# Optimization experiments

Hardware: AMD Instinct MI355X
Metric: run time of the kernel (lower is better)

Reference implementation:

```python
import jax, jax.numpy as jnp
import numpy as np

B, D, H = 4096, 64, 1024  # batch, state dim, hidden width


def setup_inputs() -> dict:
    key = jax.random.key(0)
    ks = jax.random.split(key, 4)
    def w(k, shape, fan_in):
        return (jax.random.normal(k, shape, jnp.float32) / np.float32(np.sqrt(fan_in)))
    return {
        "x": jax.random.normal(ks[0], (B, 1 + D), jnp.float32),
        "W1": w(ks[1], (D, H), D),
        "b1": jnp.zeros((H,), jnp.float32),
        "W2": w(ks[2], (H, H), H),
        "b2": jnp.zeros((H,), jnp.float32),
        "W3": w(ks[3], (H, D), H),
        "b3": jnp.zeros((D,), jnp.float32),
    }


def _mlp(z, W1, b1, W2, b2, W3, b3):
    # tanh MLP vector field: d -> h -> h -> d
    h = jnp.tanh(z @ W1 + b1)
    h = jnp.tanh(h @ W2 + b2)
    return h @ W3 + b3


def reference(x, W1, b1, W2, b2, W3, b3):
    x_in = x[:, 1:]                        # [B, D] state (col 0 is logp channel)
    f = lambda z: _mlp(z, W1, b1, W2, b2, W3, b3)
    x_out = f(x_in)                        # [B, D]

    # Exact Jacobian trace: same math as the torch per-dim autograd.grad loop,
    # expressed as D forward-mode JVPs vmapped over the identity basis.
    eye = jnp.eye(x_in.shape[1], dtype=x.dtype)

    def diag_entry(e):                     # e: [D] basis vector
        _, t = jax.jvp(f, (x_in,), (jnp.broadcast_to(e, x_in.shape),))
        return t @ e                       # [B] = J[:, i, i]

    trJ = jnp.sum(jax.vmap(diag_entry)(eye), axis=0)  # [B]

    out = jnp.concatenate([-trJ[:, None], x_out], axis=1)  # [B, 1+D]
    return out + 0.0 * x  # faithful to `+ 0 * x` in the original
```

## Files before the change

kernel.cpp:

```cpp
#include <hip/hip_runtime.h>
#include <cmath>

typedef unsigned short u16;
typedef __attribute__((ext_vector_type(8))) short s8v;
typedef __attribute__((ext_vector_type(4))) float f4v;
typedef __attribute__((ext_vector_type(16))) float f16v;

__device__ __forceinline__ u16 f2bf(float f) {
    union { float f; unsigned u; } v; v.f = f;
    unsigned r = v.u + 0x7FFFu + ((v.u >> 16) & 1u);
    return (u16)(r >> 16);
}
__device__ __forceinline__ float tanh_fast(float x) {
    float e = __builtin_amdgcn_exp2f(x * 2.88539008177792681f);
    return 1.f - 2.f * __builtin_amdgcn_rcpf(1.f + e);
}
__device__ __forceinline__ int wslot(int row, int c) {
    return ((((c >> 2) << 6) | ((c & 3) << 4) | (row & 15)) ^ c);
}
__device__ __forceinline__ size_t fragoff(int n, int k) {
    return (((size_t)(n >> 5) * 64 + (k >> 4)) * 64 + (n & 31) + (((k >> 3) & 1) << 5)) * 8 + (k & 7);
}

__launch_bounds__(256)
__global__ void cnf_prep(const float* __restrict__ x, const float* __restrict__ W1,
                         const float* __restrict__ W2, const float* __restrict__ W3,
                         u16* __restrict__ W2Tf, u16* __restrict__ VTf,
                         u16* __restrict__ xb, u16* __restrict__ W1T,
                         u16* __restrict__ W3Tf, float* __restrict__ trJ)
{
    __shared__ float w2s[32][33];
    __shared__ float w1s[64][33];
    const int a = blockIdx.x * 32;
    const int b = blockIdx.y * 32;
    const int t = threadIdx.x;

    #pragma unroll
    for (int it = 0; it < 4; ++it) {
        int idx = t + it * 256;
        w2s[idx >> 5][idx & 31] = W2[(a + (idx >> 5)) * 1024 + b + (idx & 31)];
    }
    #pragma unroll
    for (int it = 0; it < 8; ++it) {
        int idx = t + it * 256;
        w1s[idx >> 5][idx & 31] = W1[(idx >> 5) * 1024 + a + (idx & 31)];
    }
    __syncthreads();

    #pragma unroll
    for (int it = 0; it < 4; ++it) {
        int idx = t + it * 256;
        int rr = idx >> 5, cc = idx & 31;
        W2Tf[fragoff(b + rr, a + cc)] = f2bf(w2s[cc][rr]);
    }
    #pragma unroll
    for (int it = 0; it < 4; ++it) {
        int idx = t + it * 256;
        int qq = idx >> 5, pp = idx & 31;
        const float* w3row = W3 + (b + qq) * 64;
        float u = 0.f;
        #pragma unroll
        for (int i4 = 0; i4 < 16; ++i4) {
            f4v w3v = *(const f4v*)&w3row[i4 * 4];
            u += w3v[0] * w1s[i4 * 4 + 0][pp] + w3v[1] * w1s[i4 * 4 + 1][pp]
               + w3v[2] * w1s[i4 * 4 + 2][pp] + w3v[3] * w1s[i4 * 4 + 3][pp];
        }
        VTf[fragoff(b + qq, a + pp)] = f2bf(w2s[pp][qq] * u);
    }
    {
        int bid = blockIdx.y * 32 + blockIdx.x;
        int e = bid * 256 + t;
        xb[e] = f2bf(x[(e >> 6) * 65 + 1 + (e & 63)]);
    }
    if (blockIdx.y == 0) {
        int pp = t >> 3, i0 = (t & 7) * 8;
        s8v v;
        #pragma unroll
        for (int j = 0; j < 8; ++j) v[j] = (short)f2bf(w1s[i0 + j][pp]);
        *(s8v*)&W1T[(a + pp) * 64 + i0] = v;
        if (t < 128) trJ[blockIdx.x * 128 + t] = 0.f;
    }
    if (blockIdx.y == 1) {
        int idx = blockIdx.x * 256 + t;
        int n = idx & 63, k0 = (idx >> 6) * 8;
        s8v v;
        #pragma unroll
        for (int j = 0; j < 8; ++j) v[j] = (short)f2bf(W3[(k0 + j) * 64 + n]);
        *(s8v*)&W3Tf[fragoff(n, k0)] = v;
    }
}

__launch_bounds__(256)
__global__ void cnf_gemm1(const u16* __restrict__ xb, const u16* __restrict__ W1T,
                          const float* __restrict__ b1,
                          u16* __restrict__ h1, u16* __restrict__ g1)
{
    __shared__ __align__(16) u16 lds[12 * 1024];
    __shared__ __align__(16) u16 hls[128 * 64];
    __shared__ __align__(16) u16 gls[128 * 64];
    const int t = threadIdx.x;
    const int wave = t >> 6, lane = t & 63;
    const int wm = wave >> 1, wn = wave & 1;
    const int g = lane >> 4, lr = lane & 15;
    const int arow0 = blockIdx.x * 128, bcol0 = blockIdx.y * 64;

    #pragma unroll
    for (int i = 0; i < 4; ++i) {
        int ch = t + i * 256, row = ch >> 3, c = ch & 7;
        *(s8v*)&lds[(row >> 4) * 1024 + wslot(row, c) * 8] =
            *(const s8v*)&xb[(arow0 + row) * 64 + c * 8];
    }
    #pragma unroll
    for (int i = 0; i < 2; ++i) {
        int ch = t + i * 256, row = ch >> 3, c = ch & 7;
        *(s8v*)&lds[(8 + (row >> 4)) * 1024 + wslot(row, c) * 8] =
            *(const s8v*)&W1T[(bcol0 + row) * 64 + c * 8];
    }
    __syncthreads();

    f4v acc[4][2];
    #pragma unroll
    for (int mi = 0; mi < 4; ++mi)
        #pragma unroll
        for (int ni = 0; ni < 2; ++ni) acc[mi][ni] = f4v{0.f,0.f,0.f,0.f};

    #pragma unroll
    for (int ks = 0; ks < 2; ++ks) {
        const int lo = (ks * 64 + (lane ^ ((ks * 4 + g) & 7))) * 8;
        s8v af[4], bf[2];
        #pragma unroll
        for (int mi = 0; mi < 4; ++mi) af[mi] = *(const s8v*)&lds[(wm * 4 + mi) * 1024 + lo];
        #pragma unroll
        for (int ni = 0; ni < 2; ++ni) bf[ni] = *(const s8v*)&lds[(8 + wn * 2 + ni) * 1024 + lo];
        #pragma unroll
        for (int mi = 0; mi < 4; ++mi)
            #pragma unroll
            for (int ni = 0; ni < 2; ++ni)
                acc[mi][ni] = __builtin_amdgcn_mfma_f32_16x16x32_bf16(af[mi], bf[ni], acc[mi][ni], 0, 0, 0);
    }

    #pragma unroll
    for (int mi = 0; mi < 4; ++mi) {
        const int rowl = wm * 64 + mi * 16 + g * 4;
        #pragma unroll
        for (int ni = 0; ni < 2; ++ni) {
            const int coll = wn * 32 + ni * 16 + lr;
            const float bv = b1[bcol0 + coll];
            const int cc = coll >> 3, jj = coll & 7;
            #pragma unroll
            for (int r = 0; r < 4; ++r) {
                const int row = rowl + r;
                float h = tanh_fast(acc[mi][ni][r] + bv);
                int idx = row * 64 + ((cc ^ (row & 7)) << 3) + jj;
                hls[idx] = f2bf(h);
                gls[idx] = f2bf(1.f - h * h);
            }
        }
    }
    __syncthreads();

    #pragma unroll
    for (int i = 0; i < 4; ++i) {
        int id = i * 256 + t;
        int row = id >> 3, ch = id & 7;
        int src = row * 64 + ((ch ^ (row & 7)) << 3);
        size_t dst = (size_t)(arow0 + row) * 1024 + bcol0 + ch * 8;
        *(s8v*)&h1[dst] = *(const s8v*)&hls[src];
        *(s8v*)&g1[dst] = *(const s8v*)&gls[src];
    }
}

#define LOADA(dh, dg, ko) \
    do { dh = *(const s8v*)(h1p + (ko)); dg = *(const s8v*)(g1p + (ko)); } while (0)

#define LOADB(B, kkg)                                                          \
    do { _Pragma("unroll")                                                     \
         for (int _ks = 0; _ks < 2; ++_ks)                                     \
         _Pragma("unroll")                                                     \
         for (int _ni = 0; _ni < 2; ++_ni) {                                   \
             size_t _o = (((size_t)(nt0 + _ni) * 64 + (kkg) * 2 + _ks) * 64 + lane) * 8; \
             B[_ks*4 + _ni*2 + 0] = *(const s8v*)&W2Tf[_o];                    \
             B[_ks*4 + _ni*2 + 1] = *(const s8v*)&VTf[_o];                     \
         } } while (0)

#define WRITEA(sh, sg, bb)                                                     \
    do { u16* _wb = &lds[bb][0];                                               \
         *(s8v*)&_wb[sdst] = sh; *(s8v*)&_wb[4096 + sdst] = sg; } while (0)

#define MIDBODY(kt, AwH, AwG, AlH, AlG, Bc, Bn)                                \
    {                                                                          \
        if ((kt) < 30) { const int _ko = ((kt) + 2) * 32; LOADA(AlH, AlG, _ko); } \
        if ((kt) < 31) { WRITEA(AwH, AwG, ((kt) + 1) & 1); LOADB(Bn, (kt) + 1); } \
        const u16* buf = &lds[(kt) & 1][0];                                    \
        _Pragma("unroll")                                                      \
        for (int ks = 0; ks < 2; ++ks) {                                       \
            const int lp = (lane ^ ((lane >> 5) << 2) ^ (ks << 1)) * 8;        \
            const int R = wrt * 2 + ks;                                        \
            s8v a1 = *(const s8v*)&buf[R * 512 + lp];                          \
            s8v a2 = *(const s8v*)&buf[4096 + R * 512 + lp];                   \
            _Pragma("unroll")                                                  \
            for (int ni = 0; ni < 2; ++ni) {                                   \
                acc1[ni] = __builtin_amdgcn_mfma_f32_32x32x16_bf16(a1, Bc[ks*4+ni*2+0], acc1[ni], 0, 0, 0); \
                acc2[ni] = __builtin_amdgcn_mfma_f32_32x32x16_bf16(a2, Bc[ks*4+ni*2+1], acc2[ni], 0, 0, 0); \
            }                                                                  \
        }                                                                      \
        __syncthreads();                                                       \
    }

__launch_bounds__(512, 2)
__global__ void cnf_mid(const u16* __restrict__ h1, const u16* __restrict__ g1,
                        const u16* __restrict__ W2Tf, const u16* __restrict__ VTf,
                        const float* __restrict__ b2,
                        u16* __restrict__ h2f, float* __restrict__ trJ)
{
    __shared__ __align__(16) u16 lds[2][8192];

    const int t = threadIdx.x;
    const int wave = t >> 6, lane = t & 63;
    const int wrt = wave & 3;
    const int wn  = wave >> 2;
    const int arow0 = blockIdx.x * 128;
    const int ntb = blockIdx.y * 4;
    const int nt0 = ntb + wn * 2;

    const int row = t >> 2, c = t & 3;
    const int R0 = (row >> 5) * 2 + (c >> 1);
    const int L0 = (row & 31) + ((c & 1) << 5);
    const int sdst = (R0 * 64 + (L0 ^ ((L0 >> 5) << 2) ^ ((R0 & 1) << 1))) * 8;
    const u16* h1p = h1 + (size_t)(arow0 + row) * 1024 + c * 8;
    const u16* g1p = g1 + (size_t)(arow0 + row) * 1024 + c * 8;

    f16v acc1[2], acc2[2];
    #pragma unroll
    for (int ni = 0; ni < 2; ++ni)
        #pragma unroll
        for (int r = 0; r < 16; ++r) { acc1[ni][r] = 0.f; acc2[ni][r] = 0.f; }

    s8v ahA, agA, ahB, agB;
    s8v bA[8], bB[8];

    LOADA(ahA, agA, 0);
    WRITEA(ahA, agA, 0);
    LOADA(ahB, agB, 32);
    LOADB(bA, 0);
    __syncthreads();

    for (int kt2 = 0; kt2 < 16; ++kt2) {
        const int kt = kt2 * 2;
        MIDBODY(kt,     ahB, agB, ahA, agA, bA, bB);
        MIDBODY(kt + 1, ahA, agA, ahB, agB, bB, bA);
    }

    const int l31 = lane & 31, lh = lane >> 5;
    const int rt = (arow0 >> 5) + wrt;
    float tr[16];
    #pragma unroll
    for (int r = 0; r < 16; ++r) tr[r] = 0.f;
    #pragma unroll
    for (int ni = 0; ni < 2; ++ni) {
        const int q0 = (nt0 + ni) * 32;
        const float bv = b2[q0 + l31];
        const size_t hb = (((size_t)rt * 64 + ((q0 + l31) >> 4)) * 64
                           + (((l31 >> 3) & 1) << 5)) * 8 + (l31 & 7) + lh * 32;
        #pragma unroll
        for (int r = 0; r < 16; ++r) {
            float hh = tanh_fast(acc1[ni][r] + bv);
            float gg = 1.f - hh * hh;
            h2f[hb + ((r & 3) + ((r >> 2) << 3)) * 8] = f2bf(hh);
            tr[r] += acc2[ni][r] * gg;
        }
    }
    #pragma unroll
    for (int off = 1; off < 32; off <<= 1)
        #pragma unroll
        for (int r = 0; r < 16; ++r) tr[r] += __shfl_xor(tr[r], off);
    if (l31 == 0) {
        const int rowb = arow0 + wrt * 32 + lh * 4;
        #pragma unroll
        for (int r = 0; r < 16; ++r)
            atomicAdd(&trJ[rowb + (r & 3) + ((r >> 2) << 3)], tr[r]);
    }
}

__launch_bounds__(256)
__global__ void cnf_out(const u16* __restrict__ h2f, const u16* __restrict__ W3Tf,
                        const float* __restrict__ b3, const float* __restrict__ trJ,
                        float* __restrict__ out)
{
    __shared__ float red[4][32][64];
    const int t = threadIdx.x;
    const int wave = t >> 6, lane = t & 63;
    const int rt = blockIdx.x;

    f16v acc[2];
    #pragma unroll
    for (int ni = 0; ni < 2; ++ni)
        #pragma unroll
        for (int r = 0; r < 16; ++r) acc[ni][r] = 0.f;

    #pragma unroll
    for (int kki = 0; kki < 16; ++kki) {
        const int kk = wave * 16 + kki;
        s8v af = *(const s8v*)&h2f[(((size_t)rt * 64 + kk) * 64 + lane) * 8];
        #pragma unroll
        for (int ni = 0; ni < 2; ++ni) {
            s8v bf = *(const s8v*)&W3Tf[(((size_t)ni * 64 + kk) * 64 + lane) * 8];
            acc[ni] = __builtin_amdgcn_mfma_f32_32x32x16_bf16(af, bf, acc[ni], 0, 0, 0);
        }
    }
    const int l31 = lane & 31, lh = lane >> 5;
    #pragma unroll
    for (int ni = 0; ni < 2; ++ni)
        #pragma unroll
        for (int r = 0; r < 16; ++r)
            red[wave][(r & 3) + ((r >> 2) << 3) + lh * 4][ni * 32 + l31] = acc[ni][r];
    __syncthreads();

    #pragma unroll
    for (int i = 0; i < 8; ++i) {
        int o = t * 8 + i;
        int row = o >> 6, col = o & 63;
        float s = red[0][row][col] + red[1][row][col] + red[2][row][col] + red[3][row][col] + b3[col];
        out[(size_t)(rt * 32 + row) * 65 + 1 + col] = s;
    }
    if (t < 32) out[(size_t)(rt * 32 + t) * 65] = -trJ[rt * 32 + t];
}

extern "C" void kernel_launch(void* const* d_in, const int* in_sizes, int n_in,
                              void* d_out, int out_size, void* d_ws, size_t ws_size,
                              hipStream_t stream) {
    const float* x  = (const float*)d_in[0];
    const float* W1 = (const float*)d_in[1];
    const float* b1 = (const float*)d_in[2];
    const float* W2 = (const float*)d_in[3];
    const float* b2 = (const float*)d_in[4];
    const float* W3 = (const float*)d_in[5];
    const float* b3 = (const float*)d_in[6];
    float* out = (float*)d_out;

    char* ws = (char*)d_ws;
    u16*   h1b = (u16*)(ws);
    u16*   g1b = (u16*)(ws + (size_t)( 8u << 20));
    u16*   h2f = (u16*)(ws + (size_t)(16u << 20));
    u16*   W2T = (u16*)(ws + (size_t)(24u << 20));
    u16*   VTb = (u16*)(ws + (size_t)(26u << 20));
    float* trJ = (float*)(ws + (size_t)(28u << 20));
    u16*   xbb = (u16*)(ws + (size_t)(28u << 20) + 65536);
    u16*   W1T = (u16*)(ws + (size_t)(28u << 20) + 65536 + 524288);
    u16*   W3T = (u16*)(ws + (size_t)(28u << 20) + 65536 + 524288 + 131072);

    cnf_prep <<<dim3(32, 32), 256, 0, stream>>>(x, W1, W2, W3, W2T, VTb, xbb, W1T, W3T, trJ);
    cnf_gemm1<<<dim3(32, 16), 256, 0, stream>>>(xbb, W1T, b1, h1b, g1b);
    cnf_mid  <<<dim3(32, 8),  512, 0, stream>>>(h1b, g1b, W2T, VTb, b2, h2f, trJ);
    cnf_out  <<<128,          256, 0, stream>>>(h2f, W3T, b3, trJ, out);
}
```

Measured before the change: 61.54 us.

## Retile mid GEMM waves to 2 row-tiles x 1 col-tile and vectorize VT prep

In cnf_mid each wave now covers two 32-row M tiles against a single 32-column N tile, where it previously covered one M tile against two N tiles. This halves the per-wave B-fragment global loads (W2T/VT) and doubles A reads from LDS. The trace shuffle-reduce and atomics now run once per M tile, which doubles that epilogue work. Launch bounds drop to one block per SM, and the prep kernel vectorizes the VT product over 4 columns with float4 LDS reads, padding w1s to 36 columns.

Measured after the change: 55.49 us. 1.11x faster.

```diff
diff --git a/kernel.cpp b/kernel.cpp
--- a/kernel.cpp
+++ b/kernel.cpp
@@ -30,7 +30,7 @@
                          u16* __restrict__ W3Tf, float* __restrict__ trJ)
 {
     __shared__ float w2s[32][33];
-    __shared__ float w1s[64][33];
+    __shared__ __align__(16) float w1s[64][36];
     const int a = blockIdx.x * 32;
     const int b = blockIdx.y * 32;
     const int t = threadIdx.x;
@@ -53,19 +53,24 @@
         int rr = idx >> 5, cc = idx & 31;
         W2Tf[fragoff(b + rr, a + cc)] = f2bf(w2s[cc][rr]);
     }
-    #pragma unroll
-    for (int it = 0; it < 4; ++it) {
-        int idx = t + it * 256;
-        int qq = idx >> 5, pp = idx & 31;
-        const float* w3row = W3 + (b + qq) * 64;
-        float u = 0.f;
+    {
+        const int q = t >> 3, pg = t & 7;
+        const float* w3row = W3 + (b + q) * 64;
+        f4v u = f4v{0.f, 0.f, 0.f, 0.f};
         #pragma unroll
         for (int i4 = 0; i4 < 16; ++i4) {
             f4v w3v = *(const f4v*)&w3row[i4 * 4];
-            u += w3v[0] * w1s[i4 * 4 + 0][pp] + w3v[1] * w1s[i4 * 4 + 1][pp]
-               + w3v[2] * w1s[i4 * 4 + 2][pp] + w3v[3] * w1s[i4 * 4 + 3][pp];
-        }
-        VTf[fragoff(b + qq, a + pp)] = f2bf(w2s[pp][qq] * u);
+            #pragma unroll
+            for (int s = 0; s < 4; ++s) {
+                f4v wv = *(const f4v*)&w1s[i4 * 4 + s][pg * 4];
+                u += w3v[s] * wv;
+            }
+        }
+        #pragma unroll
+        for (int j = 0; j < 4; ++j) {
+            const int pp = pg * 4 + j;
+            VTf[fragoff(b + q, a + pp)] = f2bf(w2s[pp][q] * u[j]);
+        }
     }
     {
         int bid = blockIdx.y * 32 + blockIdx.x;
@@ -175,12 +180,10 @@
 
 #define LOADB(B, kkg)                                                          \
     do { _Pragma("unroll")                                                     \
-         for (int _ks = 0; _ks < 2; ++_ks)                                     \
-         _Pragma("unroll")                                                     \
-         for (int _ni = 0; _ni < 2; ++_ni) {                                   \
-             size_t _o = (((size_t)(nt0 + _ni) * 64 + (kkg) * 2 + _ks) * 64 + lane) * 8; \
-             B[_ks*4 + _ni*2 + 0] = *(const s8v*)&W2Tf[_o];                    \
-             B[_ks*4 + _ni*2 + 1] = *(const s8v*)&VTf[_o];                     \
+         for (int _ks = 0; _ks < 2; ++_ks) {                                   \
+             size_t _o = (((size_t)(ntb + wn) * 64 + (kkg) * 2 + _ks) * 64 + lane) * 8; \
+             B[_ks*2 + 0] = *(const s8v*)&W2Tf[_o];                            \
+             B[_ks*2 + 1] = *(const s8v*)&VTf[_o];                             \
          } } while (0)
 
 #define WRITEA(sh, sg, bb)                                                     \
@@ -195,19 +198,23 @@
         _Pragma("unroll")                                                      \
         for (int ks = 0; ks < 2; ++ks) {                                       \
             const int lp = (lane ^ ((lane >> 5) << 2) ^ (ks << 1)) * 8;        \
-            const int R = wrt * 2 + ks;                                        \
-            s8v a1 = *(const s8v*)&buf[R * 512 + lp];                          \
-            s8v a2 = *(const s8v*)&buf[4096 + R * 512 + lp];                   \
+            s8v a1[2], a2[2];                                                  \
             _Pragma("unroll")                                                  \
-            for (int ni = 0; ni < 2; ++ni) {                                   \
-                acc1[ni] = __builtin_amdgcn_mfma_f32_32x32x16_bf16(a1, Bc[ks*4+ni*2+0], acc1[ni], 0, 0, 0); \
-                acc2[ni] = __builtin_amdgcn_mfma_f32_32x32x16_bf16(a2, Bc[ks*4+ni*2+1], acc2[ni], 0, 0, 0); \
+            for (int mt = 0; mt < 2; ++mt) {                                   \
+                const int R = (wrt * 2 + mt) * 2 + ks;                         \
+                a1[mt] = *(const s8v*)&buf[R * 512 + lp];                      \
+                a2[mt] = *(const s8v*)&buf[4096 + R * 512 + lp];               \
+            }                                                                  \
+            _Pragma("unroll")                                                  \
+            for (int mt = 0; mt < 2; ++mt) {                                   \
+                acc1[mt] = __builtin_amdgcn_mfma_f32_32x32x16_bf16(a1[mt], Bc[ks*2+0], acc1[mt], 0, 0, 0); \
+                acc2[mt] = __builtin_amdgcn_mfma_f32_32x32x16_bf16(a2[mt], Bc[ks*2+1], acc2[mt], 0, 0, 0); \
             }                                                                  \
         }                                                                      \
         __syncthreads();                                                       \
     }
 
-__launch_bounds__(512, 2)
+__launch_bounds__(512, 1)
 __global__ void cnf_mid(const u16* __restrict__ h1, const u16* __restrict__ g1,
                         const u16* __restrict__ W2Tf, const u16* __restrict__ VTf,
                         const float* __restrict__ b2,
@@ -217,11 +224,10 @@
 
     const int t = threadIdx.x;
     const int wave = t >> 6, lane = t & 63;
-    const int wrt = wave & 3;
-    const int wn  = wave >> 2;
+    const int wrt = wave & 1;
+    const int wn  = wave >> 1;
     const int arow0 = blockIdx.x * 128;
     const int ntb = blockIdx.y * 4;
-    const int nt0 = ntb + wn * 2;
 
     const int row = t >> 2, c = t & 3;
     const int R0 = (row >> 5) * 2 + (c >> 1);
@@ -232,12 +238,12 @@
 
     f16v acc1[2], acc2[2];
     #pragma unroll
-    for (int ni = 0; ni < 2; ++ni)
-        #pragma unroll
-        for (int r = 0; r < 16; ++r) { acc1[ni][r] = 0.f; acc2[ni][r] = 0.f; }
+    for (int mt = 0; mt < 2; ++mt)
+        #pragma unroll
+        for (int r = 0; r < 16; ++r) { acc1[mt][r] = 0.f; acc2[mt][r] = 0.f; }
 
     s8v ahA, agA, ahB, agB;
-    s8v bA[8], bB[8];
+    s8v bA[4], bB[4];
 
     LOADA(ahA, agA, 0);
     WRITEA(ahA, agA, 0);
@@ -252,33 +258,31 @@
     }
 
     const int l31 = lane & 31, lh = lane >> 5;
-    const int rt = (arow0 >> 5) + wrt;
-    float tr[16];
-    #pragma unroll
-    for (int r = 0; r < 16; ++r) tr[r] = 0.f;
-    #pragma unroll
-    for (int ni = 0; ni < 2; ++ni) {
-        const int q0 = (nt0 + ni) * 32;
+    #pragma unroll
+    for (int mt = 0; mt < 2; ++mt) {
+        const int rt = (arow0 >> 5) + wrt * 2 + mt;
+        const int q0 = (ntb + wn) * 32;
         const float bv = b2[q0 + l31];
         const size_t hb = (((size_t)rt * 64 + ((q0 + l31) >> 4)) * 64
                            + (((l31 >> 3) & 1) << 5)) * 8 + (l31 & 7) + lh * 32;
+        float tr[16];
         #pragma unroll
         for (int r = 0; r < 16; ++r) {
-            float hh = tanh_fast(acc1[ni][r] + bv);
+            float hh = tanh_fast(acc1[mt][r] + bv);
             float gg = 1.f - hh * hh;
             h2f[hb + ((r & 3) + ((r >> 2) << 3)) * 8] = f2bf(hh);
-            tr[r] += acc2[ni][r] * gg;
-        }
-    }
-    #pragma unroll
-    for (int off = 1; off < 32; off <<= 1)
-        #pragma unroll
-        for (int r = 0; r < 16; ++r) tr[r] += __shfl_xor(tr[r], off);
-    if (l31 == 0) {
-        const int rowb = arow0 + wrt * 32 + lh * 4;
-        #pragma unroll
-        for (int r = 0; r < 16; ++r)
-            atomicAdd(&trJ[rowb + (r & 3) + ((r >> 2) << 3)], tr[r]);
+            tr[r] = acc2[mt][r] * gg;
+        }
+        #pragma unroll
+        for (int off = 1; off < 32; off <<= 1)
+            #pragma unroll
+            for (int r = 0; r < 16; ++r) tr[r] += __shfl_xor(tr[r], off);
+        if (l31 == 0) {
+            const int rowb = arow0 + (wrt * 2 + mt) * 32 + lh * 4;
+            #pragma unroll
+            for (int r = 0; r < 16; ++r)
+                atomicAdd(&trJ[rowb + (r & 3) + ((r >> 2) << 3)], tr[r]);
+        }
     }
 }
 
```
